# Kernel optimization log

Hardware: AMD Instinct MI355X
Metric: run time of the kernel (lower is better)

## Reference

```python
import jax, jax.numpy as jnp
import numpy as np

REG_COEF = 0.001


def setup_inputs() -> dict:
    key = jax.random.key(0)
    k1, k2, k3, k4 = jax.random.split(key, 4)
    B, K, d = 8192, 1024, 64
    q = jax.random.normal(k1, (B, d), dtype=jnp.float32)
    c = jax.random.normal(k2, (K, d), dtype=jnp.float32)
    # positive bandwidths, as produced by adjust_bandwidth (1/(2*rho^2))
    bandwidth = jax.random.uniform(k3, (K,), dtype=jnp.float32, minval=0.1, maxval=1.0)
    g_inv_c = jax.random.normal(k4, (K, d, d), dtype=jnp.float32)
    return {"q": q, "c": c, "bandwidth": bandwidth, "g_inv_c": g_inv_c}


def reference(q, c, bandwidth, g_inv_c):
    # squared euclidean distances: ||q-c||^2, computed via the expanded form
    sq_q = jnp.sum(q * q, axis=-1, keepdims=True)           # (B,1)
    sq_c = jnp.sum(c * c, axis=-1)                          # (K,)
    d2 = jnp.maximum(sq_q + sq_c[None, :] - 2.0 * (q @ c.T), 0.0)  # (B,K)
    weights = jnp.exp(-bandwidth[None, :] * d2)             # (B,K)
    g_inv = jnp.einsum('bk,kij->bij', weights, g_inv_c)     # (B,d,d)
    d = q.shape[-1]
    g_inv = g_inv + REG_COEF * jnp.eye(d, dtype=q.dtype)[None, :, :]
    return g_inv
```

## Files before the change

kernel.cpp:

```cpp
#include <hip/hip_runtime.h>
#include <hip/hip_bf16.h>

typedef __attribute__((ext_vector_type(8))) short bf16x8;
typedef __attribute__((ext_vector_type(4))) float f32x4;

#define Bsz 8192
#define Ksz 1024
#define Dsz 64
#define Nsz 4096

__device__ __forceinline__ void async_load16(const void* g, void* lds) {
    __builtin_amdgcn_global_load_lds(
        (const __attribute__((address_space(1))) void*)g,
        (__attribute__((address_space(3))) void*)lds,
        16, 0, 0);
}

__device__ __forceinline__ float bf2f(unsigned short s) {
    union { unsigned u; float f; } x;
    x.u = ((unsigned)s) << 16;
    return x.f;
}

__global__ __launch_bounds__(256) void transpose_convert(
    const float* __restrict__ G, __hip_bfloat16* __restrict__ Gt)
{
    __shared__ float tile[64][65];
    const int t = threadIdx.x;
    const int n0 = blockIdx.x * 64;
    const int k0 = blockIdx.y * 64;

    for (int i = 0; i < 4; ++i) {
        int f4 = t + 256 * i;
        int row = f4 >> 4;
        int c4  = (f4 & 15) << 2;
        float4 v = *(const float4*)&G[(size_t)(k0 + row) * Nsz + n0 + c4];
        tile[row][c4 + 0] = v.x;
        tile[row][c4 + 1] = v.y;
        tile[row][c4 + 2] = v.z;
        tile[row][c4 + 3] = v.w;
    }
    __syncthreads();
    for (int i = 0; i < 4; ++i) {
        int o = t + 256 * i;
        int rowp = o >> 4;
        int c4   = (o & 15) << 2;
        union { ushort4 u; __hip_bfloat16 h[4]; } cvt;
        cvt.h[0] = __float2bfloat16(tile[c4 + 0][rowp]);
        cvt.h[1] = __float2bfloat16(tile[c4 + 1][rowp]);
        cvt.h[2] = __float2bfloat16(tile[c4 + 2][rowp]);
        cvt.h[3] = __float2bfloat16(tile[c4 + 3][rowp]);
        *(ushort4*)&Gt[(size_t)(n0 + rowp) * Ksz + k0 + c4] = cvt.u;
    }
}

#define QSTR 72

__global__ __launch_bounds__(256) void weights_mfma(
    const float* __restrict__ q, const float* __restrict__ c,
    const float* __restrict__ bw, __hip_bfloat16* __restrict__ W)
{
    __shared__ __attribute__((aligned(16))) __hip_bfloat16 qh[128 * QSTR];
    __shared__ __attribute__((aligned(16))) __hip_bfloat16 ql[128 * QSTR];
    __shared__ __attribute__((aligned(16))) __hip_bfloat16 ch[128 * QSTR];
    __shared__ __attribute__((aligned(16))) __hip_bfloat16 cl[128 * QSTR];
    __shared__ float sqq[128];
    __shared__ float sqc[128];

    const int t  = threadIdx.x;
    const int b0 = blockIdx.x * 128;
    const int k0 = blockIdx.y * 128;

    for (int i = 0; i < 8; ++i) {
        int f4  = t + 256 * i;
        int row = f4 >> 4;
        int c4  = (f4 & 15) << 2;
        float4 v = *(const float4*)&q[(size_t)(b0 + row) * Dsz + c4];
        float4 u = *(const float4*)&c[(size_t)(k0 + row) * Dsz + c4];
        float qv[4] = {v.x, v.y, v.z, v.w};
        float cv[4] = {2.f * u.x, 2.f * u.y, 2.f * u.z, 2.f * u.w};
        union { ushort4 u4; __hip_bfloat16 h[4]; } qhh, qll, chh, cll;
        #pragma unroll
        for (int e = 0; e < 4; ++e) {
            __hip_bfloat16 hb = __float2bfloat16(qv[e]);
            qhh.h[e] = hb;
            qll.h[e] = __float2bfloat16(qv[e] - bf2f(*(unsigned short*)&hb));
            __hip_bfloat16 hc = __float2bfloat16(cv[e]);
            chh.h[e] = hc;
            cll.h[e] = __float2bfloat16(cv[e] - bf2f(*(unsigned short*)&hc));
        }
        *(ushort4*)&qh[row * QSTR + c4] = qhh.u4;
        *(ushort4*)&ql[row * QSTR + c4] = qll.u4;
        *(ushort4*)&ch[row * QSTR + c4] = chh.u4;
        *(ushort4*)&cl[row * QSTR + c4] = cll.u4;
    }
    __syncthreads();

    if (t < 128) {
        float s = 0.f;
        for (int x8 = 0; x8 < 64; x8 += 8) {
            bf16x8 h = *(const bf16x8*)&qh[t * QSTR + x8];
            bf16x8 l = *(const bf16x8*)&ql[t * QSTR + x8];
            #pragma unroll
            for (int e = 0; e < 8; ++e) {
                float v = bf2f((unsigned short)h[e]) + bf2f((unsigned short)l[e]);
                s += v * v;
            }
        }
        sqq[t] = s;
    } else {
        int r = t - 128;
        float s = 0.f;
        for (int x8 = 0; x8 < 64; x8 += 8) {
            bf16x8 h = *(const bf16x8*)&ch[r * QSTR + x8];
            bf16x8 l = *(const bf16x8*)&cl[r * QSTR + x8];
            #pragma unroll
            for (int e = 0; e < 8; ++e) {
                float v = 0.5f * (bf2f((unsigned short)h[e]) + bf2f((unsigned short)l[e]));
                s += v * v;
            }
        }
        sqc[r] = s;
    }
    __syncthreads();

    const int wave = t >> 6;
    const int lane = t & 63;
    const int wm = (wave >> 1) * 64;
    const int wn = (wave & 1) * 64;
    const int lrow = lane & 15;
    const int lk8  = (lane >> 4) << 3;

    f32x4 acc[4][4];
    for (int i = 0; i < 4; ++i)
        for (int j = 0; j < 4; ++j) acc[i][j] = (f32x4){0.f, 0.f, 0.f, 0.f};

    #pragma unroll
    for (int ks = 0; ks < 64; ks += 32) {
        bf16x8 ah[4], al[4], bh[4], bl[4];
        #pragma unroll
        for (int i = 0; i < 4; ++i) {
            int ra = (wm + i * 16 + lrow) * QSTR + ks + lk8;
            int rb = (wn + i * 16 + lrow) * QSTR + ks + lk8;
            ah[i] = *(const bf16x8*)&qh[ra];
            al[i] = *(const bf16x8*)&ql[ra];
            bh[i] = *(const bf16x8*)&ch[rb];
            bl[i] = *(const bf16x8*)&cl[rb];
        }
        #pragma unroll
        for (int i = 0; i < 4; ++i)
            #pragma unroll
            for (int j = 0; j < 4; ++j) {
                acc[i][j] = __builtin_amdgcn_mfma_f32_16x16x32_bf16(ah[i], bh[j], acc[i][j], 0, 0, 0);
                acc[i][j] = __builtin_amdgcn_mfma_f32_16x16x32_bf16(ah[i], bl[j], acc[i][j], 0, 0, 0);
                acc[i][j] = __builtin_amdgcn_mfma_f32_16x16x32_bf16(al[i], bh[j], acc[i][j], 0, 0, 0);
            }
    }

    const int crow = (lane >> 4) << 2;
    const int ccol = lane & 15;
    for (int j = 0; j < 4; ++j) {
        int k = wn + j * 16 + ccol;
        float bwv = bw[k0 + k];
        float sc  = sqc[k];
        #pragma unroll
        for (int i = 0; i < 4; ++i) {
            #pragma unroll
            for (int r = 0; r < 4; ++r) {
                int b = wm + i * 16 + crow + r;
                float d2 = fmaxf(sqq[b] + sc - acc[i][j][r], 0.f);
                W[(size_t)(b0 + b) * Ksz + (k0 + k)] = __float2bfloat16(__expf(-bwv * d2));
            }
        }
    }
}

#define TM 128
#define TN 128
#define BK 64

__global__ __launch_bounds__(256) void gemm_wg(
    const __hip_bfloat16* __restrict__ A,
    const __hip_bfloat16* __restrict__ Bt,
    float* __restrict__ C)
{
    __shared__ __attribute__((aligned(16))) __hip_bfloat16 As[TM * BK];
    __shared__ __attribute__((aligned(16))) __hip_bfloat16 Bs[TN * BK];

    const int t    = threadIdx.x;
    const int wave = t >> 6;
    const int lane = t & 63;
    const int m0 = blockIdx.y * TM;
    const int n0 = blockIdx.x * TN;

    const int wm = (wave >> 1) * 64;
    const int wn = (wave & 1) * 64;
    const int lrow = lane & 15;
    const int kg   = lane >> 4;

    f32x4 acc[4][4];
    for (int i = 0; i < 4; ++i)
        for (int j = 0; j < 4; ++j) acc[i][j] = (f32x4){0.f, 0.f, 0.f, 0.f};

    for (int k0 = 0; k0 < Ksz; k0 += BK) {
        __syncthreads();
        #pragma unroll
        for (int r = 0; r < 4; ++r) {
            int chunk = r * 256 + wave * 64 + lane;
            int row   = chunk >> 3;
            int c8    = chunk & 7;
            int g8    = c8 ^ (row & 7);
            async_load16(A  + (size_t)(m0 + row) * Ksz + k0 + g8 * 8, &As[chunk * 8]);
            async_load16(Bt + (size_t)(n0 + row) * Ksz + k0 + g8 * 8, &Bs[chunk * 8]);
        }
        __syncthreads();

        #pragma unroll
        for (int ks = 0; ks < 2; ++ks) {
            bf16x8 af[4], bfr[4];
            #pragma unroll
            for (int i = 0; i < 4; ++i) {
                int ra = wm + i * 16 + lrow;
                int ca = ((ks * 4 + kg) ^ (ra & 7)) * 8;
                af[i] = *(const bf16x8*)&As[ra * BK + ca];
                int rb = wn + i * 16 + lrow;
                int cb = ((ks * 4 + kg) ^ (rb & 7)) * 8;
                bfr[i] = *(const bf16x8*)&Bs[rb * BK + cb];
            }
            #pragma unroll
            for (int i = 0; i < 4; ++i)
                #pragma unroll
                for (int j = 0; j < 4; ++j)
                    acc[i][j] = __builtin_amdgcn_mfma_f32_16x16x32_bf16(
                        af[i], bfr[j], acc[i][j], 0, 0, 0);
        }
    }

    const int crow = (lane >> 4) << 2;
    const int ccol = lane & 15;
    for (int i = 0; i < 4; ++i) {
        for (int j = 0; j < 4; ++j) {
            int gn = n0 + wn + j * 16 + ccol;
            float diag = (gn % 65 == 0) ? 0.001f : 0.f;
            #pragma unroll
            for (int r = 0; r < 4; ++r) {
                int gm = m0 + wm + i * 16 + crow + r;
                C[(size_t)gm * Nsz + gn] = acc[i][j][r] + diag;
            }
        }
    }
}

extern "C" void kernel_launch(void* const* d_in, const int* in_sizes, int n_in,
                              void* d_out, int out_size, void* d_ws, size_t ws_size,
                              hipStream_t stream) {
    const float* q  = (const float*)d_in[0];
    const float* c  = (const float*)d_in[1];
    const float* bw = (const float*)d_in[2];
    const float* G  = (const float*)d_in[3];
    float* out = (float*)d_out;

    __hip_bfloat16* W  = (__hip_bfloat16*)d_ws;
    __hip_bfloat16* Gt = (__hip_bfloat16*)((char*)d_ws + (size_t)16 * 1024 * 1024);

    transpose_convert<<<dim3(Nsz / 64, Ksz / 64), 256, 0, stream>>>(G, Gt);
    weights_mfma<<<dim3(Bsz / 128, Ksz / 128), 256, 0, stream>>>(q, c, bw, W);
    gemm_wg<<<dim3(Nsz / TN, Bsz / TM), 256, 0, stream>>>(W, Gt, out);
}
```

Before: 226.7 us.

## Replace GEMM with 256x256 double-buffered, phase-scheduled MFMA kernel

Replaces the 128x128 single-buffered weighted-sum GEMM with a 512-thread 256x256 tile kernel. It double-buffers LDS via async global-to-LDS loads and splits each K step into four MFMA quadrants interleaved with prefetches, barriers and priority bumps. The change also swizzles the block order for L2 locality and uses nontemporal stores for the large fp32 output. It aims to overlap memory with MFMA and raise arithmetic intensity, at the cost of more LDS and registers and fragile manual waitcnt sequencing.

Result: no change. 229.1 us (+1.0%).

```diff
diff --git a/kernel.cpp b/kernel.cpp
--- a/kernel.cpp
+++ b/kernel.cpp
@@ -175,77 +175,171 @@
     }
 }
 
-#define TM 128
-#define TN 128
-#define BK 64
-
-__global__ __launch_bounds__(256) void gemm_wg(
+#define TM2 256
+#define TN2 256
+#define BK2 64
+#define NT  (Ksz / BK2)
+
+#define BAR()        __builtin_amdgcn_s_barrier()
+#define WAIT_LGKM0() asm volatile("s_waitcnt lgkmcnt(0)" ::: "memory")
+
+#define MFMA_QUAD(B, MO, NO)                                                   \
+    _Pragma("unroll")                                                          \
+    for (int ks = 0; ks < 2; ++ks)                                             \
+        _Pragma("unroll")                                                      \
+        for (int m = 0; m < 4; ++m)                                            \
+            _Pragma("unroll")                                                  \
+            for (int n = 0; n < 2; ++n)                                        \
+                acc[MO + m][NO + n] = __builtin_amdgcn_mfma_f32_16x16x32_bf16( \
+                    a[ks][m], B[ks][n], acc[MO + m][NO + n], 0, 0, 0);
+
+__global__ __launch_bounds__(512, 2) void gemm_8ph(
     const __hip_bfloat16* __restrict__ A,
     const __hip_bfloat16* __restrict__ Bt,
     float* __restrict__ C)
 {
-    __shared__ __attribute__((aligned(16))) __hip_bfloat16 As[TM * BK];
-    __shared__ __attribute__((aligned(16))) __hip_bfloat16 Bs[TN * BK];
+    __shared__ __attribute__((aligned(16))) __hip_bfloat16 As[2 * 2 * 128 * 64];
+    __shared__ __attribute__((aligned(16))) __hip_bfloat16 Bs[2 * 2 * 128 * 64];
 
     const int t    = threadIdx.x;
     const int wave = t >> 6;
     const int lane = t & 63;
-    const int m0 = blockIdx.y * TM;
-    const int n0 = blockIdx.x * TN;
-
-    const int wm = (wave >> 1) * 64;
-    const int wn = (wave & 1) * 64;
+
+    const int wg  = blockIdx.x;
+    const int swz = (wg & 7) * (512 / 8) + (wg >> 3);
+    const int bx  = swz & 15;
+    const int by  = swz >> 4;
+    const int m0  = by * TM2;
+    const int n0  = bx * TN2;
+
+    const int wm   = (wave >> 2) * 128;
+    const int wn   = (wave & 3) * 64;
     const int lrow = lane & 15;
     const int kg   = lane >> 4;
 
-    f32x4 acc[4][4];
-    for (int i = 0; i < 4; ++i)
+    f32x4 acc[8][4];
+    #pragma unroll
+    for (int i = 0; i < 8; ++i)
+        #pragma unroll
         for (int j = 0; j < 4; ++j) acc[i][j] = (f32x4){0.f, 0.f, 0.f, 0.f};
 
-    for (int k0 = 0; k0 < Ksz; k0 += BK) {
-        __syncthreads();
-        #pragma unroll
-        for (int r = 0; r < 4; ++r) {
-            int chunk = r * 256 + wave * 64 + lane;
-            int row   = chunk >> 3;
-            int c8    = chunk & 7;
-            int g8    = c8 ^ (row & 7);
-            async_load16(A  + (size_t)(m0 + row) * Ksz + k0 + g8 * 8, &As[chunk * 8]);
-            async_load16(Bt + (size_t)(n0 + row) * Ksz + k0 + g8 * 8, &Bs[chunk * 8]);
-        }
-        __syncthreads();
-
-        #pragma unroll
-        for (int ks = 0; ks < 2; ++ks) {
-            bf16x8 af[4], bfr[4];
-            #pragma unroll
-            for (int i = 0; i < 4; ++i) {
-                int ra = wm + i * 16 + lrow;
-                int ca = ((ks * 4 + kg) ^ (ra & 7)) * 8;
-                af[i] = *(const bf16x8*)&As[ra * BK + ca];
-                int rb = wn + i * 16 + lrow;
-                int cb = ((ks * 4 + kg) ^ (rb & 7)) * 8;
-                bfr[i] = *(const bf16x8*)&Bs[rb * BK + cb];
-            }
-            #pragma unroll
-            for (int i = 0; i < 4; ++i)
-                #pragma unroll
-                for (int j = 0; j < 4; ++j)
-                    acc[i][j] = __builtin_amdgcn_mfma_f32_16x16x32_bf16(
-                        af[i], bfr[j], acc[i][j], 0, 0, 0);
-        }
+    auto stageA = [&](int tt, int h) {
+        __hip_bfloat16* lds = &As[(((tt & 1) << 1) + h) * 8192];
+        const int row0 = m0 + (h << 6);
+        const int kcol = tt << 6;
+        #pragma unroll
+        for (int l = 0; l < 2; ++l) {
+            int ch   = (l << 9) + t;
+            int rl   = ch >> 3;
+            int g8   = (ch & 7) ^ (rl & 7);
+            int grow = row0 + ((rl >> 6) << 7) + (rl & 63);
+            async_load16(A + (size_t)grow * Ksz + kcol + (g8 << 3), lds + (ch << 3));
+        }
+    };
+    auto stageB = [&](int tt, int h) {
+        __hip_bfloat16* lds = &Bs[(((tt & 1) << 1) + h) * 8192];
+        const int row0 = n0 + (h << 5);
+        const int kcol = tt << 6;
+        #pragma unroll
+        for (int l = 0; l < 2; ++l) {
+            int ch   = (l << 9) + t;
+            int rl   = ch >> 3;
+            int g8   = (ch & 7) ^ (rl & 7);
+            int grow = row0 + ((rl >> 5) << 6) + (rl & 31);
+            async_load16(Bt + (size_t)grow * Ksz + kcol + (g8 << 3), lds + (ch << 3));
+        }
+    };
+
+    bf16x8 a[2][4], b0[2][2], b1[2][2];
+
+    auto readA = [&](int bb, int mh) {
+        const __hip_bfloat16* base = &As[((bb << 1) + mh) * 8192];
+        #pragma unroll
+        for (int ks = 0; ks < 2; ++ks)
+            #pragma unroll
+            for (int m = 0; m < 4; ++m) {
+                int rl = (wm >> 1) + m * 16 + lrow;
+                int cc = ((((ks << 2) + kg) ^ (rl & 7)) << 3);
+                a[ks][m] = *(const bf16x8*)&base[rl * 64 + cc];
+            }
+    };
+    auto readB = [&](bf16x8 (&b)[2][2], int bb, int nh) {
+        const __hip_bfloat16* base = &Bs[((bb << 1) + nh) * 8192];
+        #pragma unroll
+        for (int ks = 0; ks < 2; ++ks)
+            #pragma unroll
+            for (int n = 0; n < 2; ++n) {
+                int rl = (wn >> 1) + n * 16 + lrow;
+                int cc = ((((ks << 2) + kg) ^ (rl & 7)) << 3);
+                b[ks][n] = *(const bf16x8*)&base[rl * 64 + cc];
+            }
+    };
+
+    stageA(0, 0); stageA(0, 1); stageB(0, 0); stageB(0, 1);
+    stageA(1, 0); stageB(1, 0); stageB(1, 1);
+    asm volatile("s_waitcnt vmcnt(6)" ::: "memory");
+    BAR();
+
+    #pragma unroll 2
+    for (int tt = 0; tt < NT; ++tt) {
+        const int buf = tt & 1;
+
+        readA(buf, 0);
+        readB(b0, buf, 0);
+        if (tt + 1 < NT) stageA(tt + 1, 1);
+        asm volatile("s_waitcnt lgkmcnt(8)" ::: "memory");
+        BAR();
+        WAIT_LGKM0();
+        __builtin_amdgcn_s_setprio(1);
+        MFMA_QUAD(b0, 0, 0);
+        __builtin_amdgcn_s_setprio(0);
+        BAR();
+
+        readB(b1, buf, 1);
+        if (tt + 2 < NT) stageA(tt + 2, 0);
+        BAR();
+        WAIT_LGKM0();
+        __builtin_amdgcn_s_setprio(1);
+        MFMA_QUAD(b1, 0, 2);
+        __builtin_amdgcn_s_setprio(0);
+        BAR();
+
+        readA(buf, 1);
+        if (tt + 2 < NT) stageB(tt + 2, 0);
+        BAR();
+        WAIT_LGKM0();
+        __builtin_amdgcn_s_setprio(1);
+        MFMA_QUAD(b1, 4, 2);
+        __builtin_amdgcn_s_setprio(0);
+        BAR();
+
+        if (tt + 2 < NT) stageB(tt + 2, 1);
+        BAR();
+        WAIT_LGKM0();
+        __builtin_amdgcn_s_setprio(1);
+        MFMA_QUAD(b0, 4, 0);
+        __builtin_amdgcn_s_setprio(0);
+        if (tt < NT - 2) {
+            asm volatile("s_waitcnt vmcnt(6)" ::: "memory");
+        } else if (tt == NT - 2) {
+            asm volatile("s_waitcnt vmcnt(0)" ::: "memory");
+        }
+        BAR();
     }
 
     const int crow = (lane >> 4) << 2;
     const int ccol = lane & 15;
-    for (int i = 0; i < 4; ++i) {
-        for (int j = 0; j < 4; ++j) {
-            int gn = n0 + wn + j * 16 + ccol;
-            float diag = (gn % 65 == 0) ? 0.001f : 0.f;
+    #pragma unroll
+    for (int nj = 0; nj < 4; ++nj) {
+        int gn = n0 + wn + ((nj >> 1) << 5) + ((nj & 1) << 4) + ccol;
+        float diag = (gn % 65 == 0) ? 0.001f : 0.f;
+        #pragma unroll
+        for (int mi = 0; mi < 8; ++mi) {
+            int gmb = m0 + wm + ((mi >> 2) << 6) + ((mi & 3) << 4) + crow;
             #pragma unroll
             for (int r = 0; r < 4; ++r) {
-                int gm = m0 + wm + i * 16 + crow + r;
-                C[(size_t)gm * Nsz + gn] = acc[i][j][r] + diag;
+                __builtin_nontemporal_store(acc[mi][nj][r] + diag,
+                                            &C[(size_t)(gmb + r) * Nsz + gn]);
             }
         }
     }
@@ -265,5 +359,5 @@
 
     transpose_convert<<<dim3(Nsz / 64, Ksz / 64), 256, 0, stream>>>(G, Gt);
     weights_mfma<<<dim3(Bsz / 128, Ksz / 128), 256, 0, stream>>>(q, c, bw, W);
-    gemm_wg<<<dim3(Nsz / TN, Bsz / TM), 256, 0, stream>>>(W, Gt, out);
-}
+    gemm_8ph<<<dim3((Bsz / TM2) * (Nsz / TN2)), 512, 0, stream>>>(W, Gt, out);
+}
```

## Double-buffer GEMM with async LDS prefetch, 256x128 tiles and swizzled block order

Applied to the files above, without the earlier changes.

Replaces the single-buffered 128x128 bf16 GEMM with a 512-thread, 256x128-tile kernel. It double-buffers LDS with BK=32 stages and prefetches two stages ahead using vmcnt waits and raw barriers, so global loads overlap the MFMA work. It also raises MFMA priority, remaps block IDs for L2 locality, and writes output with nontemporal stores. The costs are tighter synchronisation reasoning (the vmcnt counts must match the loads issued per stage) and more LDS per block.

Result: no change. 225.1 us (-0.7%).

```diff
diff --git a/kernel.cpp b/kernel.cpp
--- a/kernel.cpp
+++ b/kernel.cpp
@@ -175,77 +175,119 @@
     }
 }
 
-#define TM 128
-#define TN 128
-#define BK 64
-
-__global__ __launch_bounds__(256) void gemm_wg(
+#define TM3 256
+#define TN3 128
+#define BK3 32
+#define NT3 32
+
+#define BAR()  __builtin_amdgcn_s_barrier()
+
+__global__ __launch_bounds__(512, 4) void gemm_2b(
     const __hip_bfloat16* __restrict__ A,
     const __hip_bfloat16* __restrict__ Bt,
     float* __restrict__ C)
 {
-    __shared__ __attribute__((aligned(16))) __hip_bfloat16 As[TM * BK];
-    __shared__ __attribute__((aligned(16))) __hip_bfloat16 Bs[TN * BK];
+    __shared__ __attribute__((aligned(16))) __hip_bfloat16 As[2 * 128 * 64];
+    __shared__ __attribute__((aligned(16))) __hip_bfloat16 Bs[2 * 64 * 64];
 
     const int t    = threadIdx.x;
     const int wave = t >> 6;
     const int lane = t & 63;
-    const int m0 = blockIdx.y * TM;
-    const int n0 = blockIdx.x * TN;
-
-    const int wm = (wave >> 1) * 64;
-    const int wn = (wave & 1) * 64;
+
+    const int wg  = blockIdx.x;
+    const int swz = (wg & 7) * 128 + (wg >> 3);
+    const int bx  = swz & 31;
+    const int by  = swz >> 5;
+    const int m0  = by * TM3;
+    const int n0  = bx * TN3;
+
+    const int wm   = (wave >> 1) * 64;
+    const int wn   = (wave & 1) * 64;
     const int lrow = lane & 15;
     const int kg   = lane >> 4;
 
     f32x4 acc[4][4];
+    #pragma unroll
     for (int i = 0; i < 4; ++i)
+        #pragma unroll
         for (int j = 0; j < 4; ++j) acc[i][j] = (f32x4){0.f, 0.f, 0.f, 0.f};
 
-    for (int k0 = 0; k0 < Ksz; k0 += BK) {
-        __syncthreads();
-        #pragma unroll
-        for (int r = 0; r < 4; ++r) {
-            int chunk = r * 256 + wave * 64 + lane;
-            int row   = chunk >> 3;
-            int c8    = chunk & 7;
-            int g8    = c8 ^ (row & 7);
-            async_load16(A  + (size_t)(m0 + row) * Ksz + k0 + g8 * 8, &As[chunk * 8]);
-            async_load16(Bt + (size_t)(n0 + row) * Ksz + k0 + g8 * 8, &Bs[chunk * 8]);
-        }
-        __syncthreads();
-
-        #pragma unroll
-        for (int ks = 0; ks < 2; ++ks) {
-            bf16x8 af[4], bfr[4];
-            #pragma unroll
-            for (int i = 0; i < 4; ++i) {
-                int ra = wm + i * 16 + lrow;
-                int ca = ((ks * 4 + kg) ^ (ra & 7)) * 8;
-                af[i] = *(const bf16x8*)&As[ra * BK + ca];
-                int rb = wn + i * 16 + lrow;
-                int cb = ((ks * 4 + kg) ^ (rb & 7)) * 8;
-                bfr[i] = *(const bf16x8*)&Bs[rb * BK + cb];
-            }
-            #pragma unroll
-            for (int i = 0; i < 4; ++i)
-                #pragma unroll
-                for (int j = 0; j < 4; ++j)
-                    acc[i][j] = __builtin_amdgcn_mfma_f32_16x16x32_bf16(
-                        af[i], bfr[j], acc[i][j], 0, 0, 0);
-        }
+    auto stage = [&](int tt) {
+        const int kc = (tt & 31) << 5;
+        __hip_bfloat16* la = &As[(tt & 1) * 8192];
+        __hip_bfloat16* lb = &Bs[(tt & 1) * 4096];
+        #pragma unroll
+        for (int l = 0; l < 2; ++l) {
+            int ch = (l << 9) + t;
+            int R  = ch >> 3;
+            int cp = (ch & 7) ^ (R & 7);
+            int grow = m0 + (R << 1) + (cp >> 2);
+            int gk   = kc + ((cp & 3) << 3);
+            async_load16(A + (size_t)grow * Ksz + gk, la + (ch << 3));
+        }
+        {
+            int ch = t;
+            int R  = ch >> 3;
+            int cp = (ch & 7) ^ (R & 7);
+            int grow = n0 + (R << 1) + (cp >> 2);
+            int gk   = kc + ((cp & 3) << 3);
+            async_load16(Bt + (size_t)grow * Ksz + gk, lb + (ch << 3));
+        }
+    };
+
+    auto ldfrag = [&](const __hip_bfloat16* base, int gr) -> bf16x8 {
+        int R  = gr >> 1;
+        int cp = (((gr & 1) << 2) + kg) ^ (R & 7);
+        return *(const bf16x8*)&base[R * 64 + cp * 8];
+    };
+
+    stage(0); stage(1);
+
+    for (int tt = 0; tt < NT3; ++tt) {
+        const int buf = tt & 1;
+
+        if (tt < NT3 - 1) {
+            asm volatile("s_waitcnt vmcnt(3)" ::: "memory");
+        } else {
+            asm volatile("s_waitcnt vmcnt(0)" ::: "memory");
+        }
+        BAR();
+
+        bf16x8 a[4], b[4];
+        #pragma unroll
+        for (int mb = 0; mb < 4; ++mb)
+            a[mb] = ldfrag(&As[buf * 8192], wm + mb * 16 + lrow);
+        #pragma unroll
+        for (int nb = 0; nb < 4; ++nb)
+            b[nb] = ldfrag(&Bs[buf * 4096], wn + nb * 16 + lrow);
+        asm volatile("s_waitcnt lgkmcnt(0)" ::: "memory");
+        BAR();
+
+        if (tt + 2 < NT3) stage(tt + 2);
+
+        __builtin_amdgcn_s_setprio(1);
+        #pragma unroll
+        for (int mb = 0; mb < 4; ++mb)
+            #pragma unroll
+            for (int nb = 0; nb < 4; ++nb)
+                acc[mb][nb] = __builtin_amdgcn_mfma_f32_16x16x32_bf16(
+                    a[mb], b[nb], acc[mb][nb], 0, 0, 0);
+        __builtin_amdgcn_s_setprio(0);
     }
 
     const int crow = (lane >> 4) << 2;
     const int ccol = lane & 15;
-    for (int i = 0; i < 4; ++i) {
-        for (int j = 0; j < 4; ++j) {
-            int gn = n0 + wn + j * 16 + ccol;
-            float diag = (gn % 65 == 0) ? 0.001f : 0.f;
+    #pragma unroll
+    for (int nb = 0; nb < 4; ++nb) {
+        int gn = n0 + wn + nb * 16 + ccol;
+        float diag = (gn % 65 == 0) ? 0.001f : 0.f;
+        #pragma unroll
+        for (int mb = 0; mb < 4; ++mb) {
+            int gmb = m0 + wm + mb * 16 + crow;
             #pragma unroll
             for (int r = 0; r < 4; ++r) {
-                int gm = m0 + wm + i * 16 + crow + r;
-                C[(size_t)gm * Nsz + gn] = acc[i][j][r] + diag;
+                __builtin_nontemporal_store(acc[mb][nb][r] + diag,
+                                            &C[(size_t)(gmb + r) * Nsz + gn]);
             }
         }
     }
@@ -265,5 +307,5 @@
 
     transpose_convert<<<dim3(Nsz / 64, Ksz / 64), 256, 0, stream>>>(G, Gt);
     weights_mfma<<<dim3(Bsz / 128, Ksz / 128), 256, 0, stream>>>(q, c, bw, W);
-    gemm_wg<<<dim3(Nsz / TN, Bsz / TM), 256, 0, stream>>>(W, Gt, out);
-}
+    gemm_2b<<<dim3((Bsz / TM3) * (Nsz / TN3)), 512, 0, stream>>>(W, Gt, out);
+}
```
